# Optimization experiments

Measured on AMD Instinct MI355X. Metric: run time of the kernel, lower is better.

The kernel has to match this reference:

```python
import math
import jax, jax.numpy as jnp
import numpy as np

B, L, D, H, DFF = 2, 2048, 1024, 16, 4096
HD = D // H
NUM_BUCKETS, MAX_DISTANCE = 32, 128


def setup_inputs() -> dict:
    key = jax.random.key(0)
    ks = jax.random.split(key, 10)
    s = 0.02
    return {
        "hidden_states": jax.random.normal(ks[0], (B, L, D), dtype=jnp.float32),
        "Wq": jax.random.normal(ks[1], (D, D), dtype=jnp.float32) * s,
        "Wk": jax.random.normal(ks[2], (D, D), dtype=jnp.float32) * s,
        "Wv": jax.random.normal(ks[3], (D, D), dtype=jnp.float32) * s,
        "Wo": jax.random.normal(ks[4], (D, D), dtype=jnp.float32) * s,
        "W1": jax.random.normal(ks[5], (D, DFF), dtype=jnp.float32) * s,
        "W2": jax.random.normal(ks[6], (DFF, D), dtype=jnp.float32) * s,
        "ln1_g": jnp.ones((D,), dtype=jnp.float32),
        "ln2_g": jnp.ones((D,), dtype=jnp.float32),
        "rel_table": jax.random.normal(ks[7], (NUM_BUCKETS, H), dtype=jnp.float32) * s,
    }


def rms_norm(x, g, eps=1e-6):
    # T5-style LayerNorm: scale only, no mean subtraction
    var = jnp.mean(jnp.square(x.astype(jnp.float32)), axis=-1, keepdims=True)
    return (x.astype(jnp.float32) * jax.lax.rsqrt(var + eps)).astype(x.dtype) * g


def relative_position_bias(seq_len, table):
    # bidirectional T5 bucket scheme, num_buckets=32, max_distance=128
    ctx = jnp.arange(seq_len)[:, None]
    mem = jnp.arange(seq_len)[None, :]
    rp = mem - ctx                                  # (L, L) int
    nb = NUM_BUCKETS // 2
    buckets = (rp > 0).astype(jnp.int32) * nb
    rpa = jnp.abs(rp)
    max_exact = nb // 2
    is_small = rpa < max_exact
    safe = jnp.maximum(rpa, 1).astype(jnp.float32)  # avoid log(0); masked by is_small
    large = max_exact + (
        jnp.log(safe / max_exact) / math.log(MAX_DISTANCE / max_exact) * (nb - max_exact)
    ).astype(jnp.int32)
    large = jnp.minimum(large, nb - 1)
    buckets = buckets + jnp.where(is_small, rpa, large)   # (L, L)
    vals = table[buckets]                                  # (L, L, H)
    return jnp.transpose(vals, (2, 0, 1))[None]            # (1, H, L, L)


def reference(hidden_states, Wq, Wk, Wv, Wo, W1, W2, ln1_g, ln2_g, rel_table):
    x = hidden_states
    b, l, d = x.shape

    # --- self-attention sublayer (pre-norm) ---
    h = rms_norm(x, ln1_g)
    q = (h @ Wq).reshape(b, l, H, HD)
    k = (h @ Wk).reshape(b, l, H, HD)
    v = (h @ Wv).reshape(b, l, H, HD)

    bias = relative_position_bias(l, rel_table)            # (1, H, L, L)
    # NOTE: source's manual attention path has NO 1/sqrt(head_dim) scaling
    scores = jnp.einsum("bqhd,bkhd->bhqk", q, k) + bias
    attn = jax.nn.softmax(scores.astype(jnp.float32), axis=-1).astype(scores.dtype)
    out = jnp.einsum("bhqk,bkhd->bqhd", attn, v).reshape(b, l, d)
    x = x + out @ Wo

    # --- feed-forward sublayer (pre-norm) ---
    h = rms_norm(x, ln2_g)
    x = x + jax.nn.relu(h @ W1) @ W2
    return x
```

## Files before the change

kernel.cpp:

```cpp
#include <hip/hip_runtime.h>
#include <hip/hip_bf16.h>
#include <math.h>

#define BDIM 1024
#define HEADS 16
#define HDIM 64
#define LSEQ 2048
#define NBATCH 2
#define DFFDIM 4096
#define QKVN 3072

typedef __bf16 bf16x8_t __attribute__((ext_vector_type(8)));
typedef float f32x4_t __attribute__((ext_vector_type(4)));

__device__ __forceinline__ ushort f2bf(float f) {
    union { __hip_bfloat16 b; ushort u; } cv;
    cv.b = __float2bfloat16(f);
    return cv.u;
}
__device__ __forceinline__ float bf2f(ushort u) {
    union { unsigned int i; float f; } cv;
    cv.i = ((unsigned int)u) << 16;
    return cv.f;
}

__global__ __launch_bounds__(256) void transpose_cvt(const float* __restrict__ W,
                                                     ushort* __restrict__ Wt,
                                                     int K, int N) {
    __shared__ ushort tile[32][33];
    int bi = blockIdx.y;
    int bj = blockIdx.x;
    int tx = threadIdx.x;
    int ty = threadIdx.y;
#pragma unroll
    for (int r = 0; r < 4; ++r) {
        int krow = bi * 32 + ty + r * 8;
        int ncol = bj * 32 + tx;
        tile[ty + r * 8][tx] = f2bf(W[(size_t)krow * N + ncol]);
    }
    __syncthreads();
#pragma unroll
    for (int r = 0; r < 4; ++r) {
        int nrow = bj * 32 + ty + r * 8;
        int kcol = bi * 32 + tx;
        Wt[(size_t)nrow * K + kcol] = tile[tx][ty + r * 8];
    }
}

__global__ __launch_bounds__(256) void transpose_cvt4(const float* __restrict__ W0,
                                                      const float* __restrict__ W1,
                                                      const float* __restrict__ W2,
                                                      const float* __restrict__ W3,
                                                      ushort* __restrict__ T0,
                                                      ushort* __restrict__ T1,
                                                      ushort* __restrict__ T2,
                                                      ushort* __restrict__ T3) {
    __shared__ ushort tile[32][33];
    const int z = blockIdx.z;
    const float* W = z == 0 ? W0 : z == 1 ? W1 : z == 2 ? W2 : W3;
    ushort* T = z == 0 ? T0 : z == 1 ? T1 : z == 2 ? T2 : T3;
    int bi = blockIdx.y, bj = blockIdx.x;
    int tx = threadIdx.x, ty = threadIdx.y;
#pragma unroll
    for (int r = 0; r < 4; ++r)
        tile[ty + r * 8][tx] = f2bf(W[(size_t)(bi * 32 + ty + r * 8) * 1024 + bj * 32 + tx]);
    __syncthreads();
#pragma unroll
    for (int r = 0; r < 4; ++r)
        T[(size_t)(bj * 32 + ty + r * 8) * 1024 + bi * 32 + tx] = tile[tx][ty + r * 8];
}

__global__ __launch_bounds__(256) void vtrans(const ushort* __restrict__ qkv,
                                              ushort* __restrict__ vT) {
    __shared__ ushort t[64][72];
    const int ktile = blockIdx.x;
    const int bh = blockIdx.y;
    const int b = bh >> 4, h = bh & 15;
    const int tid = threadIdx.x;
    const int r = tid >> 2;
    const int c0 = (tid & 3) * 16;
    const ushort* src = qkv + (size_t)(b * LSEQ + ktile * 64 + r) * QKVN + 2048 + h * HDIM + c0;
    union { bf16x8_t v; ushort s[8]; } u0, u1;
    u0.v = *(const bf16x8_t*)src;
    u1.v = *(const bf16x8_t*)(src + 8);
#pragma unroll
    for (int j = 0; j < 8; ++j) { t[r][c0 + j] = u0.s[j]; t[r][c0 + 8 + j] = u1.s[j]; }
    __syncthreads();
    const int hd = tid >> 2;
    union { bf16x8_t v; ushort s[8]; } w0, w1;
#pragma unroll
    for (int j = 0; j < 8; ++j) { w0.s[j] = t[c0 + j][hd]; w1.s[j] = t[c0 + 8 + j][hd]; }
    ushort* dst = vT + (size_t)(bh * HDIM + hd) * LSEQ + ktile * 64 + c0;
    *(bf16x8_t*)dst = w0.v;
    *(bf16x8_t*)(dst + 8) = w1.v;
}

__global__ __launch_bounds__(256) void rmsnorm_k(const float* __restrict__ x,
                                                 const float* __restrict__ g,
                                                 ushort* __restrict__ out) {
    int row = blockIdx.x;
    int t = threadIdx.x;
    int w = t >> 6, l = t & 63;
    const float4 v = reinterpret_cast<const float4*>(x + (size_t)row * BDIM)[t];
    float ss = v.x * v.x + v.y * v.y + v.z * v.z + v.w * v.w;
#pragma unroll
    for (int m = 1; m <= 32; m <<= 1) ss += __shfl_xor(ss, m);
    __shared__ float wsum[4];
    if (l == 0) wsum[w] = ss;
    __syncthreads();
    float tot = wsum[0] + wsum[1] + wsum[2] + wsum[3];
    float r = rsqrtf(tot * (1.0f / BDIM) + 1e-6f);
    const float4 gv = reinterpret_cast<const float4*>(g)[t];
    ushort4 o;
    o.x = f2bf(v.x * r * gv.x);
    o.y = f2bf(v.y * r * gv.y);
    o.z = f2bf(v.z * r * gv.z);
    o.w = f2bf(v.w * r * gv.w);
    reinterpret_cast<ushort4*>(out + (size_t)row * BDIM)[t] = o;
}

__global__ void bias_table_k(const float* __restrict__ rel, float* __restrict__ btab) {
    int idx = blockIdx.x * 256 + threadIdx.x;
    if (idx >= HEADS * 4095) return;
    int h = idx / 4095;
    int d = idx % 4095;
    int rp = d - 2047;
    int bucket = rp > 0 ? 16 : 0;
    int rpa = rp < 0 ? -rp : rp;
    if (rpa < 8) {
        bucket += rpa;
    } else {
        int large = 8 + (int)(logf((float)rpa * 0.125f) * (1.0f / logf(16.0f)) * 8.0f);
        bucket += large < 15 ? large : 15;
    }
    btab[idx] = rel[bucket * HEADS + h];
}

__global__ __launch_bounds__(256) void reduce2_k(const ushort* __restrict__ parts,
                                                 const float* __restrict__ res,
                                                 float* __restrict__ out,
                                                 size_t mn) {
    size_t i = ((size_t)blockIdx.x * 256 + threadIdx.x) * 4;
    float4 r = *(const float4*)(res + i);
    ushort4 a = *(const ushort4*)(parts + i);
    ushort4 b = *(const ushort4*)(parts + mn + i);
    float4 o;
    o.x = r.x + bf2f(a.x) + bf2f(b.x);
    o.y = r.y + bf2f(a.y) + bf2f(b.y);
    o.z = r.z + bf2f(a.z) + bf2f(b.z);
    o.w = r.w + bf2f(a.w) + bf2f(b.w);
    *(float4*)(out + i) = o;
}

__global__ __launch_bounds__(256) void reduce2_rms(const ushort* __restrict__ parts,
                                                   const float* __restrict__ res,
                                                   const float* __restrict__ g,
                                                   float* __restrict__ out,
                                                   ushort* __restrict__ hout,
                                                   size_t mn) {
    int row = blockIdx.x;
    int t = threadIdx.x;
    int w = t >> 6, l = t & 63;
    size_t i = (size_t)row * BDIM + t * 4;
    float4 r = *(const float4*)(res + i);
    ushort4 a = *(const ushort4*)(parts + i);
    ushort4 b = *(const ushort4*)(parts + mn + i);
    float4 o;
    o.x = r.x + bf2f(a.x) + bf2f(b.x);
    o.y = r.y + bf2f(a.y) + bf2f(b.y);
    o.z = r.z + bf2f(a.z) + bf2f(b.z);
    o.w = r.w + bf2f(a.w) + bf2f(b.w);
    *(float4*)(out + i) = o;
    float ss = o.x * o.x + o.y * o.y + o.z * o.z + o.w * o.w;
#pragma unroll
    for (int m = 1; m <= 32; m <<= 1) ss += __shfl_xor(ss, m);
    __shared__ float wsum[4];
    if (l == 0) wsum[w] = ss;
    __syncthreads();
    float tot = wsum[0] + wsum[1] + wsum[2] + wsum[3];
    float rr = rsqrtf(tot * (1.0f / BDIM) + 1e-6f);
    const float4 gv = reinterpret_cast<const float4*>(g)[t];
    ushort4 h;
    h.x = f2bf(o.x * rr * gv.x);
    h.y = f2bf(o.y * rr * gv.y);
    h.z = f2bf(o.z * rr * gv.z);
    h.w = f2bf(o.w * rr * gv.w);
    reinterpret_cast<ushort4*>(hout + (size_t)row * BDIM)[t] = h;
}

template <int MODE, int TM, int TN>
__global__ __launch_bounds__(256) void gemm_bt(const ushort* __restrict__ A,
                                               const ushort* __restrict__ Bt,
                                               void* Cout, const float* res,
                                               int M, int N, int K, int nbx, int nkc) {
    __shared__ __align__(16) ushort As[TM * 64];
    __shared__ __align__(16) ushort Bs[TN * 64];
    constexpr int MF = TM / 32, NF = TN / 32;
    const int nwg = gridDim.x;
    const int bid = blockIdx.x;
    const int swz = (bid & 7) * (nwg >> 3) + (bid >> 3);
    const int nxy = nwg / nkc;
    const int chunk = swz / nxy;
    const int bxy = swz % nxy;
    const int bx = bxy % nbx, by = bxy / nbx;
    const int Kc = K / nkc;
    const int kbeg = chunk * Kc;
    const int tid = threadIdx.x;
    const int w = tid >> 6, l = tid & 63;
    const int wm = w >> 1, wn = w & 1;
    const int rowA0 = by * TM;
    const int colB0 = bx * TN;
    const int lr = l >> 3;
    const int scs = ((l & 7) ^ lr) * 8;
    const int c = l & 15, gq = l >> 4;
    const int rswz = (c & 7) * 8;
    f32x4_t acc[MF][NF] = {};

    auto stage = [&](int k0) {
#pragma unroll
        for (int i = 0; i < TM / 32; ++i) {
            int r = i * 32 + w * 8;
            __builtin_amdgcn_global_load_lds(
                (const __attribute__((address_space(1))) uint32_t*)(A + (size_t)(rowA0 + r + lr) * K + kbeg + k0 + scs),
                (__attribute__((address_space(3))) uint32_t*)(&As[r * 64]), 16, 0, 0);
        }
#pragma unroll
        for (int i = 0; i < TN / 32; ++i) {
            int r = i * 32 + w * 8;
            __builtin_amdgcn_global_load_lds(
                (const __attribute__((address_space(1))) uint32_t*)(Bt + (size_t)(colB0 + r + lr) * K + kbeg + k0 + scs),
                (__attribute__((address_space(3))) uint32_t*)(&Bs[r * 64]), 16, 0, 0);
        }
    };

    const int nk = Kc >> 6;
    for (int kt = 0; kt < nk; ++kt) {
        __syncthreads();
        stage(kt << 6);
        __syncthreads();
#pragma unroll
        for (int kk = 0; kk < 2; ++kk) {
            bf16x8_t av[MF], bv[NF];
#pragma unroll
            for (int mf = 0; mf < MF; ++mf)
                av[mf] = *(const bf16x8_t*)&As[(wm * (TM / 2) + mf * 16 + c) * 64 + ((kk * 32 + gq * 8) ^ rswz)];
#pragma unroll
            for (int nf = 0; nf < NF; ++nf)
                bv[nf] = *(const bf16x8_t*)&Bs[(wn * (TN / 2) + nf * 16 + c) * 64 + ((kk * 32 + gq * 8) ^ rswz)];
#pragma unroll
            for (int mf = 0; mf < MF; ++mf)
#pragma unroll
                for (int nf = 0; nf < NF; ++nf)
                    acc[mf][nf] = __builtin_amdgcn_mfma_f32_16x16x32_bf16(av[mf], bv[nf], acc[mf][nf], 0, 0, 0);
        }
    }
#pragma unroll
    for (int mf = 0; mf < MF; ++mf) {
#pragma unroll
        for (int nf = 0; nf < NF; ++nf) {
#pragma unroll
            for (int i = 0; i < 4; ++i) {
                int row = rowA0 + wm * (TM / 2) + mf * 16 + gq * 4 + i;
                int col = colB0 + wn * (TN / 2) + nf * 16 + c;
                size_t idx = (size_t)row * N + col;
                float vv = acc[mf][nf][i];
                if (MODE == 0) {
                    ((ushort*)Cout)[idx] = f2bf(vv);
                } else if (MODE == 1) {
                    ((float*)Cout)[idx] = res[idx] + vv;
                } else if (MODE == 2) {
                    ((ushort*)Cout)[idx] = f2bf(vv > 0.f ? vv : 0.f);
                } else {
                    ((ushort*)Cout)[(size_t)chunk * M * N + idx] = f2bf(vv);
                }
            }
        }
    }
}

template <int MODE>
__global__ __launch_bounds__(512, 1) void gemm_bt8(const ushort* __restrict__ A,
                                                   const ushort* __restrict__ Bt,
                                                   void* Cout,
                                                   int M, int N, int K, int nbx) {
    __shared__ __align__(16) ushort As[2][256 * 64];
    __shared__ __align__(16) ushort Bs[2][256 * 64];
    const int nwg = gridDim.x;
    const int bid = blockIdx.x;
    const int swz = (bid & 7) * (nwg >> 3) + (bid >> 3);
    const int bx = swz % nbx, by = swz / nbx;
    const int tid = threadIdx.x;
    const int w = tid >> 6, l = tid & 63;
    const int wm = w >> 2, wn = w & 3;
    const int rowA0 = by * 256, colB0 = bx * 256;
    const int st_r = tid >> 3;
    const int scs = ((l & 7) ^ (st_r & 7)) * 8;
    const int c = l & 15, gq = l >> 4;
    const int rswz = (c & 7) * 8;
    f32x4_t acc[8][4] = {};

    auto stageChunk = [&](int buf, int k0, int q) {
        __builtin_amdgcn_global_load_lds(
            (const __attribute__((address_space(1))) uint32_t*)(A + (size_t)(rowA0 + q * 64 + st_r) * K + k0 + scs),
            (__attribute__((address_space(3))) uint32_t*)(&As[buf][(q * 64 + w * 8) * 64]), 16, 0, 0);
        __builtin_amdgcn_global_load_lds(
            (const __attribute__((address_space(1))) uint32_t*)(Bt + (size_t)(colB0 + q * 64 + st_r) * K + k0 + scs),
            (__attribute__((address_space(3))) uint32_t*)(&Bs[buf][(q * 64 + w * 8) * 64]), 16, 0, 0);
    };

    const int nk = K >> 6;
    stageChunk(0, 0, 0);
    stageChunk(0, 0, 1);
    stageChunk(0, 0, 2);
    stageChunk(0, 0, 3);
    asm volatile("s_waitcnt vmcnt(0)" ::: "memory");
    __builtin_amdgcn_s_barrier();
    __builtin_amdgcn_sched_barrier(0);

    for (int k = 0; k < nk; ++k) {
        const int cur = k & 1;
        const ushort* Ab = &As[cur][0];
        const ushort* Bb = &Bs[cur][0];
#pragma unroll
        for (int q = 0; q < 4; ++q) {
            const int mh = q >> 1, nh = q & 1;
            bf16x8_t av[4][2], bv[2][2];
#pragma unroll
            for (int mf = 0; mf < 4; ++mf)
#pragma unroll
                for (int kk = 0; kk < 2; ++kk)
                    av[mf][kk] = *(const bf16x8_t*)&Ab[(wm * 128 + mh * 64 + mf * 16 + c) * 64 + ((kk * 32 + gq * 8) ^ rswz)];
#pragma unroll
            for (int nf = 0; nf < 2; ++nf)
#pragma unroll
                for (int kk = 0; kk < 2; ++kk)
                    bv[nf][kk] = *(const bf16x8_t*)&Bb[(wn * 64 + nh * 32 + nf * 16 + c) * 64 + ((kk * 32 + gq * 8) ^ rswz)];
            if (k + 1 < nk) stageChunk(cur ^ 1, (k + 1) << 6, q);
            __builtin_amdgcn_s_barrier();
            __builtin_amdgcn_sched_barrier(0);
            __builtin_amdgcn_s_setprio(1);
#pragma unroll
            for (int kk = 0; kk < 2; ++kk)
#pragma unroll
                for (int mf = 0; mf < 4; ++mf)
#pragma unroll
                    for (int nf = 0; nf < 2; ++nf)
                        acc[mh * 4 + mf][nh * 2 + nf] = __builtin_amdgcn_mfma_f32_16x16x32_bf16(
                            av[mf][kk], bv[nf][kk], acc[mh * 4 + mf][nh * 2 + nf], 0, 0, 0);
            __builtin_amdgcn_s_setprio(0);
            if (q == 3 && k + 1 < nk)
                asm volatile("s_waitcnt vmcnt(0)" ::: "memory");
            __builtin_amdgcn_s_barrier();
            __builtin_amdgcn_sched_barrier(0);
        }
    }
#pragma unroll
    for (int am = 0; am < 8; ++am) {
#pragma unroll
        for (int an = 0; an < 4; ++an) {
#pragma unroll
            for (int i = 0; i < 4; ++i) {
                int row = rowA0 + wm * 128 + am * 16 + gq * 4 + i;
                int col = colB0 + wn * 64 + an * 16 + c;
                size_t idx = (size_t)row * N + col;
                float vv = acc[am][an][i];
                if (MODE == 0) {
                    ((ushort*)Cout)[idx] = f2bf(vv);
                } else {
                    ((ushort*)Cout)[idx] = f2bf(vv > 0.f ? vv : 0.f);
                }
            }
        }
    }
}

__global__ __launch_bounds__(512) void attn_fwd(const ushort* __restrict__ qkv,
                                                const ushort* __restrict__ vT,
                                                const float* __restrict__ btab,
                                                ushort* __restrict__ ob) {
    const int tid = threadIdx.x, w = tid >> 6, l = tid & 63;
    const int bh = blockIdx.y, b = bh >> 4, h = bh & 15;
    const int qt = blockIdx.x;
    __shared__ __align__(16) ushort Ks[2][64 * 64];
    __shared__ __align__(16) ushort Vs[2][64 * 64];
    __shared__ __align__(16) ushort Pl[8][16 * 72];
    const int q0 = qt * 128 + w * 16;
    const int c = l & 15, g = l >> 4;
    const size_t rowbase = (size_t)b * LSEQ * QKVN;
    const ushort* qp = qkv + rowbase + h * HDIM;
    const ushort* kp = qkv + rowbase + BDIM + h * HDIM;
    const ushort* vtp = vT + (size_t)bh * HDIM * LSEQ;
    const int sr = tid >> 3;
    const int scs = ((l & 7) ^ (l >> 3)) * 8;
    const float* btq4 = btab + h * 4095 + 2047 - (q0 + c) + g * 4;

    bf16x8_t aq[2];
#pragma unroll
    for (int kk = 0; kk < 2; ++kk)
        aq[kk] = *(const bf16x8_t*)(qp + (size_t)(q0 + c) * QKVN + kk * 32 + g * 8);

    float lrow = 0.f;
    f32x4_t o[4] = {};
    f32x4_t s[4];

    auto stage = [&](int buf, int key0) {
        __builtin_amdgcn_global_load_lds(
            (const __attribute__((address_space(1))) uint32_t*)(kp + (size_t)(key0 + sr) * QKVN + scs),
            (__attribute__((address_space(3))) uint32_t*)(&Ks[buf][(w * 8) * 64]), 16, 0, 0);
        __builtin_amdgcn_global_load_lds(
            (const __attribute__((address_space(1))) uint32_t*)(vtp + (size_t)sr * LSEQ + key0 + scs),
            (__attribute__((address_space(3))) uint32_t*)(&Vs[buf][(w * 8) * 64]), 16, 0, 0);
    };
    auto loadBias = [&](int key0) {
#pragma unroll
        for (int nf = 0; nf < 4; ++nf)
#pragma unroll
            for (int i = 0; i < 4; ++i)
                s[nf][i] = btq4[key0 + nf * 16 + i];
    };

    stage(0, 0);
    loadBias(0);
    int cur = 0;

    ushort* Pw = Pl[w];
    const int rswz = (c & 7) << 3;
    for (int kt = 0; kt < 32; ++kt) {
        __syncthreads();
        if (kt < 31) stage(cur ^ 1, kt * 64 + 64);
#pragma unroll
        for (int kk = 0; kk < 2; ++kk)
#pragma unroll
            for (int nf = 0; nf < 4; ++nf) {
                bf16x8_t kf = *(const bf16x8_t*)&Ks[cur][(nf * 16 + c) * 64 + ((kk * 32 + g * 8) ^ rswz)];
                s[nf] = __builtin_amdgcn_mfma_f32_16x16x32_bf16(kf, aq[kk], s[nf], 0, 0, 0);
            }
        float rs = 0.f;
        union { ushort us[4]; uint2 u2; } pk[4];
#pragma unroll
        for (int nf = 0; nf < 4; ++nf)
#pragma unroll
            for (int i = 0; i < 4; ++i) {
                float pv = __expf(s[nf][i]);
                rs += pv;
                pk[nf].us[i] = f2bf(pv);
            }
        if (kt < 31) loadBias(kt * 64 + 64);
        lrow += rs;
#pragma unroll
        for (int nf = 0; nf < 4; ++nf)
            *(uint2*)&Pw[c * 72 + nf * 16 + g * 4] = pk[nf].u2;
        bf16x8_t pa[2];
#pragma unroll
        for (int kk = 0; kk < 2; ++kk)
            pa[kk] = *(const bf16x8_t*)&Pw[c * 72 + kk * 32 + g * 8];
#pragma unroll
        for (int kk = 0; kk < 2; ++kk)
#pragma unroll
            for (int hf = 0; hf < 4; ++hf) {
                bf16x8_t vf = *(const bf16x8_t*)&Vs[cur][(hf * 16 + c) * 64 + ((kk * 32 + g * 8) ^ rswz)];
                o[hf] = __builtin_amdgcn_mfma_f32_16x16x32_bf16(vf, pa[kk], o[hf], 0, 0, 0);
            }
        cur ^= 1;
    }
    lrow += __shfl_xor(lrow, 16);
    lrow += __shfl_xor(lrow, 32);
    const float inv = 1.f / lrow;
    ushort* orow = ob + (size_t)(b * LSEQ + q0 + c) * BDIM + h * HDIM + g * 4;
#pragma unroll
    for (int hf = 0; hf < 4; ++hf) {
        ushort4 ov;
        ov.x = f2bf(o[hf][0] * inv);
        ov.y = f2bf(o[hf][1] * inv);
        ov.z = f2bf(o[hf][2] * inv);
        ov.w = f2bf(o[hf][3] * inv);
        *(ushort4*)(orow + hf * 16) = ov;
    }
}

extern "C" void kernel_launch(void* const* d_in, const int* in_sizes, int n_in,
                              void* d_out, int out_size, void* d_ws, size_t ws_size,
                              hipStream_t stream) {
    const float* x   = (const float*)d_in[0];
    const float* Wq  = (const float*)d_in[1];
    const float* Wk  = (const float*)d_in[2];
    const float* Wv  = (const float*)d_in[3];
    const float* Wo  = (const float*)d_in[4];
    const float* W1  = (const float*)d_in[5];
    const float* W2  = (const float*)d_in[6];
    const float* g1  = (const float*)d_in[7];
    const float* g2  = (const float*)d_in[8];
    const float* rel = (const float*)d_in[9];
    float* out = (float*)d_out;

    char* ws = (char*)d_ws;
    const size_t MB = 1024 * 1024;
    ushort* wqkvT = (ushort*)(ws + 0 * MB);
    ushort* woT   = (ushort*)(ws + 6 * MB);
    ushort* w1T   = (ushort*)(ws + 8 * MB);
    ushort* w2T   = (ushort*)(ws + 16 * MB);
    float*  btab  = (float*)(ws + 24 * MB);
    ushort* hbuf  = (ushort*)(ws + 25 * MB);
    ushort* qkvb  = (ushort*)(ws + 33 * MB);
    ushort* woP   = (ushort*)(ws + 33 * MB);
    ushort* f1b   = (ushort*)(ws + 33 * MB);
    ushort* vTb   = (ushort*)(ws + 57 * MB);
    ushort* w2P   = (ushort*)(ws + 0 * MB);
    (void)in_sizes; (void)n_in; (void)out_size; (void)ws_size;

    const size_t MN = (size_t)4096 * 1024;
    dim3 tb(32, 8);
    transpose_cvt4<<<dim3(32, 32, 4), tb, 0, stream>>>(Wq, Wk, Wv, Wo,
        wqkvT, wqkvT + 1024 * 1024, wqkvT + 2048 * 1024, woT);
    transpose_cvt<<<dim3(128, 32), tb, 0, stream>>>(W1, w1T, 1024, 4096);
    transpose_cvt<<<dim3(32, 128), tb, 0, stream>>>(W2, w2T, 4096, 1024);
    bias_table_k<<<256, 256, 0, stream>>>(rel, btab);

    rmsnorm_k<<<4096, 256, 0, stream>>>(x, g1, hbuf);
    gemm_bt<0, 128, 128><<<768, 256, 0, stream>>>(hbuf, wqkvT, qkvb, nullptr, 4096, QKVN, 1024, 24, 1);
    vtrans<<<dim3(32, 32), 256, 0, stream>>>(qkvb, vTb);
    attn_fwd<<<dim3(16, 32), 512, 0, stream>>>(qkvb, vTb, btab, hbuf);
    gemm_bt<3, 128, 128><<<512, 256, 0, stream>>>(hbuf, woT, woP, nullptr, 4096, 1024, 1024, 8, 2);
    reduce2_rms<<<4096, 256, 0, stream>>>(woP, x, g2, out, hbuf, MN);
    gemm_bt8<2><<<256, 512, 0, stream>>>(hbuf, w1T, f1b, 4096, DFFDIM, 1024, 16);
    gemm_bt<3, 128, 128><<<512, 256, 0, stream>>>(f1b, w2T, w2P, nullptr, 4096, 1024, 4096, 8, 2);
    reduce2_k<<<4096, 256, 0, stream>>>(w2P, out, out, MN);
}
```

Baseline: 229.1 us.

## Use 256x256 split-K pipelined GEMM for Wo and W2 projections

The Wo and W2 projections move from the 128x128 gemm_bt with 2-way split-K to the 256x256 double-buffered gemm_bt8 kernel with 4-way split-K, which writes bf16 partials into two buffers. The reduction kernels now sum four partials instead of two. The aim is better operand reuse and pipelining from the large-tile kernel while keeping 256 workgroups to fill the CUs. In exchange there is more partial-sum traffic, an extra bf16 rounding step, and Wo runs with only 256 K per chunk, so its pipeline is short.

```diff
diff --git a/kernel.cpp b/kernel.cpp
--- a/kernel.cpp
+++ b/kernel.cpp
@@ -136,23 +136,27 @@
     btab[idx] = rel[bucket * HEADS + h];
 }
 
-__global__ __launch_bounds__(256) void reduce2_k(const ushort* __restrict__ parts,
+__global__ __launch_bounds__(256) void reduce4_k(const ushort* __restrict__ p01,
+                                                 const ushort* __restrict__ p23,
                                                  const float* __restrict__ res,
                                                  float* __restrict__ out,
                                                  size_t mn) {
     size_t i = ((size_t)blockIdx.x * 256 + threadIdx.x) * 4;
     float4 r = *(const float4*)(res + i);
-    ushort4 a = *(const ushort4*)(parts + i);
-    ushort4 b = *(const ushort4*)(parts + mn + i);
+    ushort4 a = *(const ushort4*)(p01 + i);
+    ushort4 b = *(const ushort4*)(p01 + mn + i);
+    ushort4 c = *(const ushort4*)(p23 + i);
+    ushort4 d = *(const ushort4*)(p23 + mn + i);
     float4 o;
-    o.x = r.x + bf2f(a.x) + bf2f(b.x);
-    o.y = r.y + bf2f(a.y) + bf2f(b.y);
-    o.z = r.z + bf2f(a.z) + bf2f(b.z);
-    o.w = r.w + bf2f(a.w) + bf2f(b.w);
+    o.x = r.x + bf2f(a.x) + bf2f(b.x) + bf2f(c.x) + bf2f(d.x);
+    o.y = r.y + bf2f(a.y) + bf2f(b.y) + bf2f(c.y) + bf2f(d.y);
+    o.z = r.z + bf2f(a.z) + bf2f(b.z) + bf2f(c.z) + bf2f(d.z);
+    o.w = r.w + bf2f(a.w) + bf2f(b.w) + bf2f(c.w) + bf2f(d.w);
     *(float4*)(out + i) = o;
 }
 
-__global__ __launch_bounds__(256) void reduce2_rms(const ushort* __restrict__ parts,
+__global__ __launch_bounds__(256) void reduce4_rms(const ushort* __restrict__ p01,
+                                                   const ushort* __restrict__ p23,
                                                    const float* __restrict__ res,
                                                    const float* __restrict__ g,
                                                    float* __restrict__ out,
@@ -163,13 +167,15 @@
     int w = t >> 6, l = t & 63;
     size_t i = (size_t)row * BDIM + t * 4;
     float4 r = *(const float4*)(res + i);
-    ushort4 a = *(const ushort4*)(parts + i);
-    ushort4 b = *(const ushort4*)(parts + mn + i);
+    ushort4 a = *(const ushort4*)(p01 + i);
+    ushort4 b = *(const ushort4*)(p01 + mn + i);
+    ushort4 c = *(const ushort4*)(p23 + i);
+    ushort4 d = *(const ushort4*)(p23 + mn + i);
     float4 o;
-    o.x = r.x + bf2f(a.x) + bf2f(b.x);
-    o.y = r.y + bf2f(a.y) + bf2f(b.y);
-    o.z = r.z + bf2f(a.z) + bf2f(b.z);
-    o.w = r.w + bf2f(a.w) + bf2f(b.w);
+    o.x = r.x + bf2f(a.x) + bf2f(b.x) + bf2f(c.x) + bf2f(d.x);
+    o.y = r.y + bf2f(a.y) + bf2f(b.y) + bf2f(c.y) + bf2f(d.y);
+    o.z = r.z + bf2f(a.z) + bf2f(b.z) + bf2f(c.z) + bf2f(d.z);
+    o.w = r.w + bf2f(a.w) + bf2f(b.w) + bf2f(c.w) + bf2f(d.w);
     *(float4*)(out + i) = o;
     float ss = o.x * o.x + o.y * o.y + o.z * o.z + o.w * o.w;
 #pragma unroll
@@ -191,11 +197,91 @@
 template <int MODE, int TM, int TN>
 __global__ __launch_bounds__(256) void gemm_bt(const ushort* __restrict__ A,
                                                const ushort* __restrict__ Bt,
-                                               void* Cout, const float* res,
-                                               int M, int N, int K, int nbx, int nkc) {
+                                               void* Cout,
+                                               int M, int N, int K, int nbx) {
     __shared__ __align__(16) ushort As[TM * 64];
     __shared__ __align__(16) ushort Bs[TN * 64];
     constexpr int MF = TM / 32, NF = TN / 32;
+    const int nwg = gridDim.x;
+    const int bid = blockIdx.x;
+    const int swz = (bid & 7) * (nwg >> 3) + (bid >> 3);
+    const int bx = swz % nbx, by = swz / nbx;
+    const int tid = threadIdx.x;
+    const int w = tid >> 6, l = tid & 63;
+    const int wm = w >> 1, wn = w & 1;
+    const int rowA0 = by * TM;
+    const int colB0 = bx * TN;
+    const int lr = l >> 3;
+    const int scs = ((l & 7) ^ lr) * 8;
+    const int c = l & 15, gq = l >> 4;
+    const int rswz = (c & 7) * 8;
+    f32x4_t acc[MF][NF] = {};
+
+    auto stage = [&](int k0) {
+#pragma unroll
+        for (int i = 0; i < TM / 32; ++i) {
+            int r = i * 32 + w * 8;
+            __builtin_amdgcn_global_load_lds(
+                (const __attribute__((address_space(1))) uint32_t*)(A + (size_t)(rowA0 + r + lr) * K + k0 + scs),
+                (__attribute__((address_space(3))) uint32_t*)(&As[r * 64]), 16, 0, 0);
+        }
+#pragma unroll
+        for (int i = 0; i < TN / 32; ++i) {
+            int r = i * 32 + w * 8;
+            __builtin_amdgcn_global_load_lds(
+                (const __attribute__((address_space(1))) uint32_t*)(Bt + (size_t)(colB0 + r + lr) * K + k0 + scs),
+                (__attribute__((address_space(3))) uint32_t*)(&Bs[r * 64]), 16, 0, 0);
+        }
+    };
+
+    const int nk = K >> 6;
+    for (int kt = 0; kt < nk; ++kt) {
+        __syncthreads();
+        stage(kt << 6);
+        __syncthreads();
+#pragma unroll
+        for (int kk = 0; kk < 2; ++kk) {
+            bf16x8_t av[MF], bv[NF];
+#pragma unroll
+            for (int mf = 0; mf < MF; ++mf)
+                av[mf] = *(const bf16x8_t*)&As[(wm * (TM / 2) + mf * 16 + c) * 64 + ((kk * 32 + gq * 8) ^ rswz)];
+#pragma unroll
+            for (int nf = 0; nf < NF; ++nf)
+                bv[nf] = *(const bf16x8_t*)&Bs[(wn * (TN / 2) + nf * 16 + c) * 64 + ((kk * 32 + gq * 8) ^ rswz)];
+#pragma unroll
+            for (int mf = 0; mf < MF; ++mf)
+#pragma unroll
+                for (int nf = 0; nf < NF; ++nf)
+                    acc[mf][nf] = __builtin_amdgcn_mfma_f32_16x16x32_bf16(av[mf], bv[nf], acc[mf][nf], 0, 0, 0);
+        }
+    }
+#pragma unroll
+    for (int mf = 0; mf < MF; ++mf) {
+#pragma unroll
+        for (int nf = 0; nf < NF; ++nf) {
+#pragma unroll
+            for (int i = 0; i < 4; ++i) {
+                int row = rowA0 + wm * (TM / 2) + mf * 16 + gq * 4 + i;
+                int col = colB0 + wn * (TN / 2) + nf * 16 + c;
+                size_t idx = (size_t)row * N + col;
+                float vv = acc[mf][nf][i];
+                if (MODE == 0) {
+                    ((ushort*)Cout)[idx] = f2bf(vv);
+                } else {
+                    ((ushort*)Cout)[idx] = f2bf(vv > 0.f ? vv : 0.f);
+                }
+            }
+        }
+    }
+}
+
+template <int MODE>
+__global__ __launch_bounds__(512, 1) void gemm_bt8(const ushort* __restrict__ A,
+                                                   const ushort* __restrict__ Bt,
+                                                   void* Cout, void* Cout2,
+                                                   int M, int N, int K, int nbx, int nkc) {
+    __shared__ __align__(16) ushort As[2][256 * 64];
+    __shared__ __align__(16) ushort Bs[2][256 * 64];
     const int nwg = gridDim.x;
     const int bid = blockIdx.x;
     const int swz = (bid & 7) * (nwg >> 3) + (bid >> 3);
@@ -207,90 +293,6 @@
     const int kbeg = chunk * Kc;
     const int tid = threadIdx.x;
     const int w = tid >> 6, l = tid & 63;
-    const int wm = w >> 1, wn = w & 1;
-    const int rowA0 = by * TM;
-    const int colB0 = bx * TN;
-    const int lr = l >> 3;
-    const int scs = ((l & 7) ^ lr) * 8;
-    const int c = l & 15, gq = l >> 4;
-    const int rswz = (c & 7) * 8;
-    f32x4_t acc[MF][NF] = {};
-
-    auto stage = [&](int k0) {
-#pragma unroll
-        for (int i = 0; i < TM / 32; ++i) {
-            int r = i * 32 + w * 8;
-            __builtin_amdgcn_global_load_lds(
-                (const __attribute__((address_space(1))) uint32_t*)(A + (size_t)(rowA0 + r + lr) * K + kbeg + k0 + scs),
-                (__attribute__((address_space(3))) uint32_t*)(&As[r * 64]), 16, 0, 0);
-        }
-#pragma unroll
-        for (int i = 0; i < TN / 32; ++i) {
-            int r = i * 32 + w * 8;
-            __builtin_amdgcn_global_load_lds(
-                (const __attribute__((address_space(1))) uint32_t*)(Bt + (size_t)(colB0 + r + lr) * K + kbeg + k0 + scs),
-                (__attribute__((address_space(3))) uint32_t*)(&Bs[r * 64]), 16, 0, 0);
-        }
-    };
-
-    const int nk = Kc >> 6;
-    for (int kt = 0; kt < nk; ++kt) {
-        __syncthreads();
-        stage(kt << 6);
-        __syncthreads();
-#pragma unroll
-        for (int kk = 0; kk < 2; ++kk) {
-            bf16x8_t av[MF], bv[NF];
-#pragma unroll
-            for (int mf = 0; mf < MF; ++mf)
-                av[mf] = *(const bf16x8_t*)&As[(wm * (TM / 2) + mf * 16 + c) * 64 + ((kk * 32 + gq * 8) ^ rswz)];
-#pragma unroll
-            for (int nf = 0; nf < NF; ++nf)
-                bv[nf] = *(const bf16x8_t*)&Bs[(wn * (TN / 2) + nf * 16 + c) * 64 + ((kk * 32 + gq * 8) ^ rswz)];
-#pragma unroll
-            for (int mf = 0; mf < MF; ++mf)
-#pragma unroll
-                for (int nf = 0; nf < NF; ++nf)
-                    acc[mf][nf] = __builtin_amdgcn_mfma_f32_16x16x32_bf16(av[mf], bv[nf], acc[mf][nf], 0, 0, 0);
-        }
-    }
-#pragma unroll
-    for (int mf = 0; mf < MF; ++mf) {
-#pragma unroll
-        for (int nf = 0; nf < NF; ++nf) {
-#pragma unroll
-            for (int i = 0; i < 4; ++i) {
-                int row = rowA0 + wm * (TM / 2) + mf * 16 + gq * 4 + i;
-                int col = colB0 + wn * (TN / 2) + nf * 16 + c;
-                size_t idx = (size_t)row * N + col;
-                float vv = acc[mf][nf][i];
-                if (MODE == 0) {
-                    ((ushort*)Cout)[idx] = f2bf(vv);
-                } else if (MODE == 1) {
-                    ((float*)Cout)[idx] = res[idx] + vv;
-                } else if (MODE == 2) {
-                    ((ushort*)Cout)[idx] = f2bf(vv > 0.f ? vv : 0.f);
-                } else {
-                    ((ushort*)Cout)[(size_t)chunk * M * N + idx] = f2bf(vv);
-                }
-            }
-        }
-    }
-}
-
-template <int MODE>
-__global__ __launch_bounds__(512, 1) void gemm_bt8(const ushort* __restrict__ A,
-                                                   const ushort* __restrict__ Bt,
-                                                   void* Cout,
-                                                   int M, int N, int K, int nbx) {
-    __shared__ __align__(16) ushort As[2][256 * 64];
-    __shared__ __align__(16) ushort Bs[2][256 * 64];
-    const int nwg = gridDim.x;
-    const int bid = blockIdx.x;
-    const int swz = (bid & 7) * (nwg >> 3) + (bid >> 3);
-    const int bx = swz % nbx, by = swz / nbx;
-    const int tid = threadIdx.x;
-    const int w = tid >> 6, l = tid & 63;
     const int wm = w >> 2, wn = w & 3;
     const int rowA0 = by * 256, colB0 = bx * 256;
     const int st_r = tid >> 3;
@@ -301,14 +303,14 @@
 
     auto stageChunk = [&](int buf, int k0, int q) {
         __builtin_amdgcn_global_load_lds(
-            (const __attribute__((address_space(1))) uint32_t*)(A + (size_t)(rowA0 + q * 64 + st_r) * K + k0 + scs),
+            (const __attribute__((address_space(1))) uint32_t*)(A + (size_t)(rowA0 + q * 64 + st_r) * K + kbeg + k0 + scs),
             (__attribute__((address_space(3))) uint32_t*)(&As[buf][(q * 64 + w * 8) * 64]), 16, 0, 0);
         __builtin_amdgcn_global_load_lds(
-            (const __attribute__((address_space(1))) uint32_t*)(Bt + (size_t)(colB0 + q * 64 + st_r) * K + k0 + scs),
+            (const __attribute__((address_space(1))) uint32_t*)(Bt + (size_t)(colB0 + q * 64 + st_r) * K + kbeg + k0 + scs),
             (__attribute__((address_space(3))) uint32_t*)(&Bs[buf][(q * 64 + w * 8) * 64]), 16, 0, 0);
     };
 
-    const int nk = K >> 6;
+    const int nk = Kc >> 6;
     stageChunk(0, 0, 0);
     stageChunk(0, 0, 1);
     stageChunk(0, 0, 2);
@@ -354,6 +356,11 @@
             __builtin_amdgcn_sched_barrier(0);
         }
     }
+    ushort* dst;
+    if (MODE == 3)
+        dst = (ushort*)(chunk < 2 ? Cout : Cout2) + (size_t)(chunk & 1) * M * N;
+    else
+        dst = (ushort*)Cout;
 #pragma unroll
     for (int am = 0; am < 8; ++am) {
 #pragma unroll
@@ -364,10 +371,10 @@
                 int col = colB0 + wn * 64 + an * 16 + c;
                 size_t idx = (size_t)row * N + col;
                 float vv = acc[am][an][i];
-                if (MODE == 0) {
-                    ((ushort*)Cout)[idx] = f2bf(vv);
+                if (MODE == 2) {
+                    dst[idx] = f2bf(vv > 0.f ? vv : 0.f);
                 } else {
-                    ((ushort*)Cout)[idx] = f2bf(vv > 0.f ? vv : 0.f);
+                    dst[idx] = f2bf(vv);
                 }
             }
         }
@@ -505,7 +512,8 @@
     ushort* woP   = (ushort*)(ws + 33 * MB);
     ushort* f1b   = (ushort*)(ws + 33 * MB);
     ushort* vTb   = (ushort*)(ws + 57 * MB);
-    ushort* w2P   = (ushort*)(ws + 0 * MB);
+    ushort* w2P0  = (ushort*)(ws + 0 * MB);
+    ushort* w2P1  = (ushort*)(ws + 65 * MB);
     (void)in_sizes; (void)n_in; (void)out_size; (void)ws_size;
 
     const size_t MN = (size_t)4096 * 1024;
@@ -517,12 +525,12 @@
     bias_table_k<<<256, 256, 0, stream>>>(rel, btab);
 
     rmsnorm_k<<<4096, 256, 0, stream>>>(x, g1, hbuf);
-    gemm_bt<0, 128, 128><<<768, 256, 0, stream>>>(hbuf, wqkvT, qkvb, nullptr, 4096, QKVN, 1024, 24, 1);
+    gemm_bt<0, 128, 128><<<768, 256, 0, stream>>>(hbuf, wqkvT, qkvb, 4096, QKVN, 1024, 24);
     vtrans<<<dim3(32, 32), 256, 0, stream>>>(qkvb, vTb);
     attn_fwd<<<dim3(16, 32), 512, 0, stream>>>(qkvb, vTb, btab, hbuf);
-    gemm_bt<3, 128, 128><<<512, 256, 0, stream>>>(hbuf, woT, woP, nullptr, 4096, 1024, 1024, 8, 2);
-    reduce2_rms<<<4096, 256, 0, stream>>>(woP, x, g2, out, hbuf, MN);
-    gemm_bt8<2><<<256, 512, 0, stream>>>(hbuf, w1T, f1b, 4096, DFFDIM, 1024, 16);
-    gemm_bt<3, 128, 128><<<512, 256, 0, stream>>>(f1b, w2T, w2P, nullptr, 4096, 1024, 4096, 8, 2);
-    reduce2_k<<<4096, 256, 0, stream>>>(w2P, out, out, MN);
-}
+    gemm_bt8<3><<<256, 512, 0, stream>>>(hbuf, woT, woP, woP + 2 * MN, 4096, 1024, 1024, 4, 4);
+    reduce4_rms<<<4096, 256, 0, stream>>>(woP, woP + 2 * MN, x, g2, out, hbuf, MN);
+    gemm_bt8<2><<<256, 512, 0, stream>>>(hbuf, w1T, f1b, nullptr, 4096, DFFDIM, 1024, 16, 1);
+    gemm_bt8<3><<<256, 512, 0, stream>>>(f1b, w2T, w2P0, w2P1, 4096, 1024, 4096, 4, 4);
+    reduce4_k<<<4096, 256, 0, stream>>>(w2P0, w2P1, out, out, MN);
+}
```

Measured after the change: 237.6 us. 1.04x slower.

## Fuse V transpose into QKV GEMM epilogue and front-load gemm_bt8 prefetch

Applied to the files above, without the earlier changes.

The QKV projection GEMM gets a new epilogue mode that writes the V columns straight into the transposed vT layout, with four consecutive keys packed per store, and skips writing them to the row-major buffer. This removes the separate vtrans kernel launch and its extra read and write of V. Separately, the 8-wave GEMM now issues all next-tile staging loads during the first two quarter-steps instead of spreading them across all four, so global loads start earlier at the cost of burstier register and VMEM pressure.

```diff
diff --git a/kernel.cpp b/kernel.cpp
--- a/kernel.cpp
+++ b/kernel.cpp
@@ -68,31 +68,6 @@
 #pragma unroll
     for (int r = 0; r < 4; ++r)
         T[(size_t)(bj * 32 + ty + r * 8) * 1024 + bi * 32 + tx] = tile[tx][ty + r * 8];
-}
-
-__global__ __launch_bounds__(256) void vtrans(const ushort* __restrict__ qkv,
-                                              ushort* __restrict__ vT) {
-    __shared__ ushort t[64][72];
-    const int ktile = blockIdx.x;
-    const int bh = blockIdx.y;
-    const int b = bh >> 4, h = bh & 15;
-    const int tid = threadIdx.x;
-    const int r = tid >> 2;
-    const int c0 = (tid & 3) * 16;
-    const ushort* src = qkv + (size_t)(b * LSEQ + ktile * 64 + r) * QKVN + 2048 + h * HDIM + c0;
-    union { bf16x8_t v; ushort s[8]; } u0, u1;
-    u0.v = *(const bf16x8_t*)src;
-    u1.v = *(const bf16x8_t*)(src + 8);
-#pragma unroll
-    for (int j = 0; j < 8; ++j) { t[r][c0 + j] = u0.s[j]; t[r][c0 + 8 + j] = u1.s[j]; }
-    __syncthreads();
-    const int hd = tid >> 2;
-    union { bf16x8_t v; ushort s[8]; } w0, w1;
-#pragma unroll
-    for (int j = 0; j < 8; ++j) { w0.s[j] = t[c0 + j][hd]; w1.s[j] = t[c0 + 8 + j][hd]; }
-    ushort* dst = vT + (size_t)(bh * HDIM + hd) * LSEQ + ktile * 64 + c0;
-    *(bf16x8_t*)dst = w0.v;
-    *(bf16x8_t*)(dst + 8) = w1.v;
 }
 
 __global__ __launch_bounds__(256) void rmsnorm_k(const float* __restrict__ x,
@@ -192,6 +167,7 @@
 __global__ __launch_bounds__(256) void gemm_bt(const ushort* __restrict__ A,
                                                const ushort* __restrict__ Bt,
                                                void* Cout, const float* res,
+                                               ushort* __restrict__ vtb,
                                                int M, int N, int K, int nbx, int nkc) {
     __shared__ __align__(16) ushort As[TM * 64];
     __shared__ __align__(16) ushort Bs[TN * 64];
@@ -254,6 +230,26 @@
                     acc[mf][nf] = __builtin_amdgcn_mfma_f32_16x16x32_bf16(av[mf], bv[nf], acc[mf][nf], 0, 0, 0);
         }
     }
+    if (MODE == 4 && colB0 >= 2048) {
+#pragma unroll
+        for (int mf = 0; mf < MF; ++mf) {
+#pragma unroll
+            for (int nf = 0; nf < NF; ++nf) {
+                int col = colB0 + wn * (TN / 2) + nf * 16 + c;
+                int v = col - 2048;
+                int hh = v >> 6, hd = v & 63;
+                int row0 = rowA0 + wm * (TM / 2) + mf * 16 + gq * 4;
+                int bb = row0 >> 11, key = row0 & 2047;
+                ushort4 ov;
+                ov.x = f2bf(acc[mf][nf][0]);
+                ov.y = f2bf(acc[mf][nf][1]);
+                ov.z = f2bf(acc[mf][nf][2]);
+                ov.w = f2bf(acc[mf][nf][3]);
+                *(ushort4*)(vtb + ((size_t)((bb * 16 + hh) * 64 + hd)) * 2048 + key) = ov;
+            }
+        }
+        return;
+    }
 #pragma unroll
     for (int mf = 0; mf < MF; ++mf) {
 #pragma unroll
@@ -264,7 +260,7 @@
                 int col = colB0 + wn * (TN / 2) + nf * 16 + c;
                 size_t idx = (size_t)row * N + col;
                 float vv = acc[mf][nf][i];
-                if (MODE == 0) {
+                if (MODE == 0 || MODE == 4) {
                     ((ushort*)Cout)[idx] = f2bf(vv);
                 } else if (MODE == 1) {
                     ((float*)Cout)[idx] = res[idx] + vv;
@@ -335,7 +331,10 @@
 #pragma unroll
                 for (int kk = 0; kk < 2; ++kk)
                     bv[nf][kk] = *(const bf16x8_t*)&Bb[(wn * 64 + nh * 32 + nf * 16 + c) * 64 + ((kk * 32 + gq * 8) ^ rswz)];
-            if (k + 1 < nk) stageChunk(cur ^ 1, (k + 1) << 6, q);
+            if (k + 1 < nk) {
+                if (q == 0) { stageChunk(cur ^ 1, (k + 1) << 6, 0); stageChunk(cur ^ 1, (k + 1) << 6, 1); }
+                else if (q == 1) { stageChunk(cur ^ 1, (k + 1) << 6, 2); stageChunk(cur ^ 1, (k + 1) << 6, 3); }
+            }
             __builtin_amdgcn_s_barrier();
             __builtin_amdgcn_sched_barrier(0);
             __builtin_amdgcn_s_setprio(1);
@@ -364,10 +363,10 @@
                 int col = colB0 + wn * 64 + an * 16 + c;
                 size_t idx = (size_t)row * N + col;
                 float vv = acc[am][an][i];
-                if (MODE == 0) {
+                if (MODE == 2) {
+                    ((ushort*)Cout)[idx] = f2bf(vv > 0.f ? vv : 0.f);
+                } else {
                     ((ushort*)Cout)[idx] = f2bf(vv);
-                } else {
-                    ((ushort*)Cout)[idx] = f2bf(vv > 0.f ? vv : 0.f);
                 }
             }
         }
@@ -517,12 +516,11 @@
     bias_table_k<<<256, 256, 0, stream>>>(rel, btab);
 
     rmsnorm_k<<<4096, 256, 0, stream>>>(x, g1, hbuf);
-    gemm_bt<0, 128, 128><<<768, 256, 0, stream>>>(hbuf, wqkvT, qkvb, nullptr, 4096, QKVN, 1024, 24, 1);
-    vtrans<<<dim3(32, 32), 256, 0, stream>>>(qkvb, vTb);
+    gemm_bt<4, 128, 128><<<768, 256, 0, stream>>>(hbuf, wqkvT, qkvb, nullptr, vTb, 4096, QKVN, 1024, 24, 1);
     attn_fwd<<<dim3(16, 32), 512, 0, stream>>>(qkvb, vTb, btab, hbuf);
-    gemm_bt<3, 128, 128><<<512, 256, 0, stream>>>(hbuf, woT, woP, nullptr, 4096, 1024, 1024, 8, 2);
+    gemm_bt<3, 128, 128><<<512, 256, 0, stream>>>(hbuf, woT, woP, nullptr, nullptr, 4096, 1024, 1024, 8, 2);
     reduce2_rms<<<4096, 256, 0, stream>>>(woP, x, g2, out, hbuf, MN);
     gemm_bt8<2><<<256, 512, 0, stream>>>(hbuf, w1T, f1b, 4096, DFFDIM, 1024, 16);
-    gemm_bt<3, 128, 128><<<512, 256, 0, stream>>>(f1b, w2T, w2P, nullptr, 4096, 1024, 4096, 8, 2);
+    gemm_bt<3, 128, 128><<<512, 256, 0, stream>>>(f1b, w2T, w2P, nullptr, nullptr, 4096, 1024, 4096, 8, 2);
     reduce2_k<<<4096, 256, 0, stream>>>(w2P, out, out, MN);
 }
```

After: 226.1 us. Within noise of the previous version (-1.3%).
